# Kernel optimization log

Measured on AMD Instinct MI355X. Metric: run time of the kernel, lower is better.

## Reference

```python
import jax, jax.numpy as jnp
import numpy as np
from jax import lax

H = W = 200          # feature map size
STRIDE = 16
IMG_H = IMG_W = H * STRIDE  # 3200
C = 512
A = 9                # 3 scales x 3 aspect ratios
K_PRE = 1000         # pre-NMS topk (hardcoded in module)
K_POST = 100         # post-NMS keep (hardcoded in module)
IOU_TH = 0.7


def make_anchors():
    scales = jnp.array([128.0, 256.0, 512.0], dtype=jnp.float32)
    ratios = jnp.array([0.5, 1.0, 2.0], dtype=jnp.float32)
    hr = jnp.sqrt(ratios)                      # (3,)
    wr = 1.0 / hr
    ws = (wr[:, None] * scales[None, :]).reshape(-1)   # (9,)
    hs = (hr[:, None] * scales[None, :]).reshape(-1)
    base = jnp.stack([-ws / 2, -hs / 2, ws / 2, hs / 2], axis=1)  # (9,4)
    sx = jnp.arange(W, dtype=jnp.float32) * STRIDE
    sy = jnp.arange(H, dtype=jnp.float32) * STRIDE
    gy, gx = jnp.meshgrid(sy, sx, indexing='ij')
    shifts = jnp.stack([gx, gy, gx, gy], axis=-1).reshape(-1, 4)  # (H*W,4)
    return (shifts[:, None, :] + base[None, :, :]).reshape(-1, 4)  # (H*W*A,4)


def decode(anchors, deltas):
    w = anchors[:, 2] - anchors[:, 0]
    h = anchors[:, 3] - anchors[:, 1]
    cx = anchors[:, 0] + 0.5 * w
    cy = anchors[:, 1] + 0.5 * h
    px = deltas[:, 0] * w + cx
    py = deltas[:, 1] * h + cy
    pw = jnp.exp(deltas[:, 2]) * w
    ph = jnp.exp(deltas[:, 3]) * h
    return jnp.stack([px - 0.5 * pw, py - 0.5 * ph, px + 0.5 * pw, py + 0.5 * ph], axis=1)


def clamp_boxes(b):
    return jnp.stack([
        jnp.clip(b[:, 0], 0.0, IMG_W), jnp.clip(b[:, 1], 0.0, IMG_H),
        jnp.clip(b[:, 2], 0.0, IMG_W), jnp.clip(b[:, 3], 0.0, IMG_H)], axis=1)


def nms_keep(boxes, thr):
    # boxes (K_PRE,4) already sorted by descending score (topk output order)
    x1, y1, x2, y2 = boxes[:, 0], boxes[:, 1], boxes[:, 2], boxes[:, 3]
    areas = (x2 - x1) * (y2 - y1)
    idx = jnp.arange(K_PRE)

    def body(i, keep):
        iw = jnp.clip(jnp.minimum(x2[i], x2) - jnp.maximum(x1[i], x1), 0.0)
        ih = jnp.clip(jnp.minimum(y2[i], y2) - jnp.maximum(y1[i], y1), 0.0)
        inter = iw * ih
        iou = inter / (areas[i] + areas - inter)
        supp = (iou > thr) & (idx > i) & keep[i]
        return keep & jnp.logical_not(supp)

    return lax.fori_loop(0, K_PRE, body, jnp.ones(K_PRE, dtype=bool))


def rpn_forward(feat, conv_w, conv_b, cls_w, cls_b, reg_w, reg_b):
    dn = ('NCHW', 'OIHW', 'NCHW')
    x = lax.conv_general_dilated(feat, conv_w, (1, 1), 'SAME', dimension_numbers=dn)
    x = jax.nn.relu(x + conv_b[None, :, None, None])
    cls = lax.conv_general_dilated(x, cls_w, (1, 1), 'SAME', dimension_numbers=dn) + cls_b[None, :, None, None]
    reg = lax.conv_general_dilated(x, reg_w, (1, 1), 'SAME', dimension_numbers=dn) + reg_b[None, :, None, None]
    # (1,A,H,W) -> (H*W*A,)
    cls_logits = cls.transpose(0, 2, 3, 1).reshape(-1)
    # (1,A*4,H,W) -> (H*W*A,4)
    deltas = reg.reshape(1, A, 4, H, W).transpose(0, 3, 4, 1, 2).reshape(-1, 4)
    anchors = make_anchors()
    proposals = decode(anchors, deltas)
    scores = jax.nn.sigmoid(cls_logits)
    top_sc, top_idx = lax.top_k(scores, K_PRE)           # sorted descending
    props = clamp_boxes(proposals[top_idx])
    keep = lax.stop_gradient(nms_keep(props, IOU_TH))    # NMS decision is non-diff
    # kept indices, in score order (stable sort puts kept first, preserving order)
    order = jnp.argsort(jnp.where(keep, 0, 1), stable=True)[:K_POST]
    valid = jnp.arange(K_POST) < jnp.sum(keep)
    out_boxes = jnp.where(valid[:, None], props[order], 0.0)
    out_scores = jnp.where(valid, top_sc[order], 0.0)
    return out_boxes, out_scores


def setup_inputs() -> dict:
    key = jax.random.key(0)
    ks = jax.random.split(key, 7)
    s = 0.02
    return {
        'feat': jax.random.normal(ks[0], (1, C, H, W), dtype=jnp.float32),
        'conv_w': jax.random.normal(ks[1], (C, C, 3, 3), dtype=jnp.float32) * s,
        'conv_b': jnp.zeros((C,), dtype=jnp.float32),
        'cls_w': jax.random.normal(ks[2], (A, C, 1, 1), dtype=jnp.float32) * s,
        'cls_b': jnp.zeros((A,), dtype=jnp.float32),
        'reg_w': jax.random.normal(ks[3], (A * 4, C, 1, 1), dtype=jnp.float32) * s,
        'reg_b': jnp.zeros((A * 4,), dtype=jnp.float32),
    }


def reference(feat, conv_w, conv_b, cls_w, cls_b, reg_w, reg_b):
    return rpn_forward(feat, conv_w, conv_b, cls_w, cls_b, reg_w, reg_b)
```

## Files before the change

kernel.cpp:

```cpp
#include <hip/hip_runtime.h>
#include <stdint.h>

static constexpr int H_ = 200, W_ = 200, HW_ = 40000;
static constexpr int C_ = 512;
static constexpr int NANCH = 360000;
static constexpr int KPRE = 1000;
static constexpr int KPOST = 100;
static constexpr int KSEL = 1400;
static constexpr int PXCAP = 4096;
static constexpr int KSPLIT = 8;
static constexpr int FT = 212;
static constexpr int FP = 202;

typedef __attribute__((ext_vector_type(8))) short bf16x8;
typedef __attribute__((ext_vector_type(4))) float f32x4;

__device__ inline ushort f2bf(float f) {
    unsigned u = __float_as_uint(f);
    u += 0x7FFFu + ((u >> 16) & 1u);
    return (ushort)(u >> 16);
}
__device__ inline float bf2f(ushort h) { return __uint_as_float(((unsigned)h) << 16); }

typedef const __attribute__((address_space(1))) uint32_t gas_u32;
typedef __attribute__((address_space(3))) uint32_t las_u32;
__device__ __forceinline__ void gload_lds16(const void* g, void* l) {
    __builtin_amdgcn_global_load_lds((gas_u32*)(uintptr_t)g, (las_u32*)(uintptr_t)l, 16, 0, 0);
}

__global__ void k_zero_u32(unsigned* __restrict__ p, int n) {
    int i = blockIdx.x * 256 + threadIdx.x;
    if (i < n) p[i] = 0u;
}

__global__ void k_zero_border_t(ushort* __restrict__ feat_t) {
    int t = blockIdx.x * 256 + threadIdx.x;
    int total = 4944 * 64;
    if (t >= total) return;
    int px = t >> 6, part = t & 63;
    int y, x;
    if (px < 2544) { int ri = px / 212; x = px - ri * 212; y = (ri == 0) ? 0 : 200 + ri; }
    else { int q = px - 2544; int r12 = q / 12; int c = q - r12 * 12; y = 1 + r12; x = (c == 0) ? 0 : 200 + c; }
    uint4 z = {0u, 0u, 0u, 0u};
    *(uint4*)&feat_t[((size_t)y * FT + x) * 512 + part * 8] = z;
}

__global__ void k_zero_border_px(float* __restrict__ feat_px) {
    int t = blockIdx.x * 256 + threadIdx.x;
    int total = 804 * 128;
    if (t >= total) return;
    int px = t >> 7, part = t & 127;
    int y, x;
    if (px < 202)      { y = 0;   x = px; }
    else if (px < 404) { y = 201; x = px - 202; }
    else if (px < 604) { x = 0;   y = 1 + (px - 404); }
    else               { x = 201; y = 1 + (px - 604); }
    float4 z = {0.f, 0.f, 0.f, 0.f};
    *(float4*)&feat_px[((size_t)y * FP + x) * 512 + part * 4] = z;
}

__global__ void k_feat_t(const float* __restrict__ feat, ushort* __restrict__ feat_t) {
    __shared__ ushort lt[32 * 8 * 33];
    int x0 = blockIdx.x * 32, y0 = blockIdx.y * 8, ci0 = blockIdx.z * 32;
    int tid = threadIdx.x;
    for (int u = tid; u < 8192; u += 256) {
        int ciL = u >> 8, rem = u & 255;
        int yy = rem >> 5, xx = rem & 31;
        int x = x0 + xx;
        float v = (x < W_) ? feat[(size_t)(ci0 + ciL) * HW_ + (y0 + yy) * W_ + x] : 0.f;
        lt[(ciL * 8 + yy) * 33 + xx] = f2bf(v);
    }
    __syncthreads();
    for (int u = tid; u < 1024; u += 256) {
        int pxu = u >> 2, part = u & 3;
        int yy = pxu >> 5, xx = pxu & 31;
        if (x0 + xx >= W_) continue;
        ushort tmp[8];
#pragma unroll
        for (int k = 0; k < 8; ++k) tmp[k] = lt[((part * 8 + k) * 8 + yy) * 33 + xx];
        *(uint4*)&feat_t[((size_t)(y0 + yy + 1) * FT + (x0 + xx + 1)) * 512 + ci0 + part * 8] =
            *(const uint4*)&tmp[0];
    }
}

__global__ void k_feat_px(const float* __restrict__ feat, float* __restrict__ feat_px) {
    __shared__ float lt[32 * 8 * 33];
    int x0 = blockIdx.x * 32, y0 = blockIdx.y * 8, ci0 = blockIdx.z * 32;
    int tid = threadIdx.x;
    for (int u = tid; u < 8192; u += 256) {
        int ciL = u >> 8, rem = u & 255;
        int yy = rem >> 5, xx = rem & 31;
        int x = x0 + xx;
        float v = (x < W_) ? feat[(size_t)(ci0 + ciL) * HW_ + (y0 + yy) * W_ + x] : 0.f;
        lt[(ciL * 8 + yy) * 33 + xx] = v;
    }
    __syncthreads();
    for (int u = tid; u < 1024; u += 256) {
        int pxu = u >> 2, part = u & 3;
        int yy = pxu >> 5, xx = pxu & 31;
        if (x0 + xx >= W_) continue;
        float tmp[8];
#pragma unroll
        for (int k = 0; k < 8; ++k) tmp[k] = lt[((part * 8 + k) * 8 + yy) * 33 + xx];
        float* dst = &feat_px[((size_t)(y0 + yy + 1) * FP + (x0 + xx + 1)) * 512 + ci0 + part * 8];
        *(float4*)&dst[0] = *(const float4*)&tmp[0];
        *(float4*)&dst[4] = *(const float4*)&tmp[4];
    }
}

__global__ void k_wt_t(const float* __restrict__ conv_w, ushort* __restrict__ wt_t) {
    int i = blockIdx.x * 256 + threadIdx.x;
    if (i >= 9 * 512 * 512) return;
    int tap = i >> 18;
    int rem = i & 262143;
    int co = rem >> 9, ci = rem & 511;
    wt_t[i] = f2bf(conv_w[((size_t)co * 512 + ci) * 9 + tap]);
}

__global__ void k_wt_ex(const float* __restrict__ conv_w, float* __restrict__ wt_ex) {
    __shared__ float t[32][33];
    int kb = blockIdx.x * 32;
    int cb = blockIdx.y * 32;
    int lx = threadIdx.x, ly = threadIdx.y;
    int tap = kb >> 9, ci0 = kb & 511;
    for (int r = ly; r < 32; r += 8)
        t[r][lx] = conv_w[((size_t)(cb + r) * 512 + ci0 + lx) * 9 + tap];
    __syncthreads();
    for (int r = ly; r < 32; r += 8)
        wt_ex[(size_t)(kb + r) * 512 + cb + lx] = t[lx][r];
}

__global__ __launch_bounds__(256)
__attribute__((amdgpu_waves_per_eu(2, 4)))
void k_conv3_mfma(const ushort* __restrict__ feat_t, const ushort* __restrict__ wt_t,
                  const float* __restrict__ bias, ushort* __restrict__ xab) {
    __shared__ ushort halo[18 * 18 * 32];
    __shared__ ushort wtile[9 * 64 * 32];
    int b = blockIdx.x;
    int cot = b & 7;
    int tile = b >> 3;
    int xt = tile % 13, yt = tile / 13;
    int x0 = xt * 16, y0 = yt * 16;
    int co0 = cot * 64;
    int tid = threadIdx.x;
    int lane = tid & 63, wid = tid >> 6;
    int l15 = lane & 15, l4 = lane >> 4;

    f32x4 acc[4][4];
#pragma unroll
    for (int i = 0; i < 4; ++i)
#pragma unroll
        for (int j = 0; j < 4; ++j) acc[i][j] = (f32x4){0.f, 0.f, 0.f, 0.f};

    for (int ch = 0; ch < 16; ++ch) {
        int ci0 = ch * 32;
        __syncthreads();
        for (int u = tid; u < 1296; u += 256) {
            int p = u >> 2, q = u & 3;
            int r = p / 18, c = p - r * 18;
            const ushort* src = feat_t + ((size_t)(y0 + r) * FT + (x0 + c)) * 512 + ci0 + q * 8;
            gload_lds16(src, &halo[(u & ~63) * 8]);
        }
        for (int u = tid; u < 2304; u += 256) {
            int row = u >> 2, q = u & 3;
            int tap = row >> 6, co = row & 63;
            const ushort* src = wt_t + ((size_t)(tap * 512 + co0 + co)) * 512 + ci0 + q * 8;
            gload_lds16(src, &wtile[(u & ~63) * 8]);
        }
        __syncthreads();
#pragma unroll
        for (int tap = 0; tap < 9; ++tap) {
            int th = tap / 3, tw = tap - th * 3;
            bf16x8 af[4], bf[4];
#pragma unroll
            for (int pi = 0; pi < 4; ++pi)
                af[pi] = *(const bf16x8*)&halo[((wid * 4 + pi + th) * 18 + (l15 + tw)) * 32 + l4 * 8];
#pragma unroll
            for (int cj = 0; cj < 4; ++cj)
                bf[cj] = *(const bf16x8*)&wtile[(tap * 64 + cj * 16 + l15) * 32 + l4 * 8];
#pragma unroll
            for (int pi = 0; pi < 4; ++pi)
#pragma unroll
                for (int cj = 0; cj < 4; ++cj)
                    acc[pi][cj] = __builtin_amdgcn_mfma_f32_16x16x32_bf16(af[pi], bf[cj], acc[pi][cj], 0, 0, 0);
        }
    }

    float bv[4];
#pragma unroll
    for (int cj = 0; cj < 4; ++cj) bv[cj] = bias[co0 + cj * 16 + l15];
#pragma unroll
    for (int pi = 0; pi < 4; ++pi) {
        int yy = y0 + wid * 4 + pi;
        if (yy >= H_) continue;
#pragma unroll
        for (int cj = 0; cj < 4; ++cj) {
            int co = co0 + cj * 16 + l15;
#pragma unroll
            for (int r = 0; r < 4; ++r) {
                int xx = x0 + l4 * 4 + r;
                if (xx < W_) {
                    float v = acc[pi][cj][r] + bv[cj];
                    xab[((size_t)(yy * W_ + xx)) * 512 + co] = f2bf(v > 0.f ? v : 0.f);
                }
            }
        }
    }
}

__global__ void k_cls(const ushort* __restrict__ xab, const float* __restrict__ cls_w,
                      const float* __restrict__ cls_b, float* __restrict__ scores) {
    __shared__ float wl[9 * 512];
    int tid = threadIdx.x;
    for (int t = tid; t < 4608; t += 256) wl[t] = cls_w[t];
    __syncthreads();
    int l = tid & 63, w = tid >> 6;
    int pbase = blockIdx.x * 64 + w * 16;
    for (int u = 0; u < 16; ++u) {
        int px = pbase + u;
        float xv[8];
#pragma unroll
        for (int k = 0; k < 8; ++k) xv[k] = bf2f(xab[(size_t)px * 512 + k * 64 + l]);
#pragma unroll
        for (int a = 0; a < 9; ++a) {
            float s = 0.f;
#pragma unroll
            for (int k = 0; k < 8; ++k) s = fmaf(xv[k], wl[a * 512 + k * 64 + l], s);
#pragma unroll
            for (int o = 32; o > 0; o >>= 1) s += __shfl_down(s, o);
            if (l == 0) scores[(size_t)px * 9 + a] = 1.f / (1.f + expf(-(s + cls_b[a])));
        }
    }
}

__global__ void k_hist1_lds(const float* __restrict__ scores, unsigned* __restrict__ hist) {
    __shared__ unsigned h[16384];
    int tid = threadIdx.x;
    for (int j = tid; j < 16384; j += 256) h[j] = 0u;
    __syncthreads();
    int stride = gridDim.x * 256;
    for (int i = blockIdx.x * 256 + tid; i < NANCH; i += stride)
        atomicAdd(&h[(__float_as_uint(scores[i]) >> 16) & 16383], 1u);
    __syncthreads();
    for (int j = tid; j < 16384; j += 256) {
        unsigned v = h[j];
        if (v) atomicAdd(&hist[j], v);
    }
}

__global__ void k_find_thr(const unsigned* __restrict__ hist, unsigned* __restrict__ meta,
                           int mode, int Kwant) {
    __shared__ unsigned csum[1024];
    int t = threadIdx.x;
    unsigned base = (mode == 0) ? 0u : meta[1];
    unsigned s = 0;
    for (int b = 0; b < 64; ++b) s += hist[t * 64 + b];
    csum[t] = s;
    __syncthreads();
    for (int off = 1; off < 1024; off <<= 1) {
        unsigned add = (t + off < 1024) ? csum[t + off] : 0u;
        __syncthreads();
        csum[t] += add;
        __syncthreads();
    }
    unsigned run = base + ((t < 1023) ? csum[t + 1] : 0u);
    for (int b = 63; b >= 0; --b) {
        unsigned h = hist[t * 64 + b];
        if (run < (unsigned)Kwant && run + h >= (unsigned)Kwant) {
            if (mode == 0) {
                meta[0] = (unsigned)(t * 64 + b);
                meta[1] = run;
            } else {
                meta[2] = (meta[0] << 16) | (unsigned)(t * 64 + b);
                meta[3] = run;
                meta[4] = (unsigned)Kwant - run;
            }
            break;
        }
        run += h;
    }
}

__global__ void k_collect_cand(const float* __restrict__ scores, const unsigned* __restrict__ meta,
                               unsigned* __restrict__ flags) {
    int i = blockIdx.x * 256 + threadIdx.x;
    if (i >= NANCH) return;
    if ((__float_as_uint(scores[i]) >> 16) >= meta[0]) flags[i / 9] = 1u;
}

__global__ void k_px_compact(unsigned* __restrict__ flags, unsigned* __restrict__ meta,
                             unsigned* __restrict__ px_list) {
    int px = blockIdx.x * 256 + threadIdx.x;
    if (px >= HW_) return;
    if (flags[px]) {
        unsigned s = atomicAdd(&meta[10], 1u);
        if (s < (unsigned)PXCAP) { px_list[s] = (unsigned)px; flags[px] = s + 1u; }
        else flags[px] = 0u;
    }
}

__global__ __attribute__((amdgpu_waves_per_eu(2, 4)))
void k_exact_gemm(const float* __restrict__ feat_px, const float* __restrict__ wt_ex,
                  const unsigned* __restrict__ meta, const unsigned* __restrict__ px_list,
                  float* __restrict__ xpart) {
    int npx = (int)meta[10]; if (npx > PXCAP) npx = PXCAP;
    int pb = blockIdx.x;
    if (pb * 64 >= npx) return;
    int cot = blockIdx.y;
    int kz = blockIdx.z;
    __shared__ float A[32][68];
    __shared__ float B[32][68];
    __shared__ int plist[64];
    int tid = threadIdx.x;
    int co0 = cot * 64;
    if (tid < 64) {
        int slot = pb * 64 + tid;
        plist[tid] = (slot < npx) ? (int)px_list[slot] : (int)px_list[0];
    }
    int tcog = tid >> 4;
    int tpxg = tid & 15;
    float acc[4][4];
#pragma unroll
    for (int i = 0; i < 4; ++i)
#pragma unroll
        for (int j = 0; j < 4; ++j) acc[i][j] = 0.f;
    int kbase = kz * 576;
    for (int kc = 0; kc < 18; ++kc) {
        int k0 = kbase + kc * 32;
        int tap = k0 >> 9, ci0c = k0 & 511;
        int th = tap / 3, tw = tap - th * 3;
        __syncthreads();
        for (int u = tid; u < 512; u += 256) {
            int k = u >> 4, cp = (u & 15) * 4;
            *(float4*)&A[k][cp] = *(const float4*)&wt_ex[(size_t)(k0 + k) * 512 + co0 + cp];
        }
        for (int u = tid; u < 512; u += 256) {
            int s = u >> 3, part = u & 7;
            int px = plist[s];
            int y = px / W_, x = px - y * W_;
            float4 v = *(const float4*)&feat_px[((size_t)(y + th) * FP + (x + tw)) * 512 + ci0c + part * 4];
            B[part * 4 + 0][s] = v.x; B[part * 4 + 1][s] = v.y;
            B[part * 4 + 2][s] = v.z; B[part * 4 + 3][s] = v.w;
        }
        __syncthreads();
#pragma unroll 4
        for (int k = 0; k < 32; ++k) {
            float wv[4], pv[4];
            *(float4*)&wv[0] = *(const float4*)&A[k][tcog * 4];
            *(float4*)&pv[0] = *(const float4*)&B[k][tpxg * 4];
#pragma unroll
            for (int i = 0; i < 4; ++i)
#pragma unroll
                for (int j = 0; j < 4; ++j) acc[i][j] = fmaf(wv[i], pv[j], acc[i][j]);
        }
    }
#pragma unroll
    for (int j = 0; j < 4; ++j) {
        int slot = pb * 64 + tpxg * 4 + j;
        if (slot >= npx) continue;
        float tmp[4];
#pragma unroll
        for (int i = 0; i < 4; ++i) tmp[i] = acc[i][j];
        *(float4*)&xpart[((size_t)kz * PXCAP + slot) * 512 + co0 + tcog * 4] = *(float4*)&tmp[0];
    }
}

__global__ void k_exact_reduce(const float* __restrict__ xpart, const float* __restrict__ bias,
                               const unsigned* __restrict__ meta, float* __restrict__ xex) {
    int npx = (int)meta[10]; if (npx > PXCAP) npx = PXCAP;
    int idx = blockIdx.x * 256 + threadIdx.x;
    int slot = idx >> 9, co = idx & 511;
    if (slot >= npx) return;
    float v = 0.f;
#pragma unroll
    for (int kz = 0; kz < KSPLIT; ++kz)
        v += xpart[((size_t)kz * PXCAP + slot) * 512 + co];
    v += bias[co];
    xex[(size_t)slot * 512 + co] = v > 0.f ? v : 0.f;
}

__global__ void k_exact_scores(const float* __restrict__ xex, const float* __restrict__ cls_w,
                               const float* __restrict__ cls_b, const unsigned* __restrict__ meta,
                               float* __restrict__ scores_ex) {
    int slot = blockIdx.x;
    int npx = (int)meta[10]; if (npx > PXCAP) npx = PXCAP;
    if (slot >= npx) return;
    int l = threadIdx.x;
    float xv[8];
#pragma unroll
    for (int k = 0; k < 8; ++k) xv[k] = xex[(size_t)slot * 512 + k * 64 + l];
#pragma unroll
    for (int a = 0; a < 9; ++a) {
        float s = 0.f;
#pragma unroll
        for (int k = 0; k < 8; ++k) s = fmaf(xv[k], cls_w[a * 512 + k * 64 + l], s);
#pragma unroll
        for (int o = 32; o > 0; o >>= 1) s += __shfl_down(s, o);
        if (l == 0) scores_ex[slot * 9 + a] = 1.f / (1.f + expf(-(s + cls_b[a])));
    }
}

__global__ void k_hist1_ex_lds(const float* __restrict__ scores_ex, const unsigned* __restrict__ meta,
                               unsigned* __restrict__ hist) {
    __shared__ unsigned h[16384];
    int npx = (int)meta[10]; if (npx > PXCAP) npx = PXCAP;
    int n = npx * 9;
    int tid = threadIdx.x;
    for (int j = tid; j < 16384; j += 256) h[j] = 0u;
    __syncthreads();
    for (int i = blockIdx.x * 256 + tid; i < n; i += 32 * 256)
        atomicAdd(&h[(__float_as_uint(scores_ex[i]) >> 16) & 16383], 1u);
    __syncthreads();
    for (int j = tid; j < 16384; j += 256) {
        unsigned v = h[j];
        if (v) atomicAdd(&hist[j], v);
    }
}

__global__ void k_hist2_ex(const float* __restrict__ scores_ex, const unsigned* __restrict__ meta,
                           const unsigned* __restrict__ meta_ex, unsigned* __restrict__ hist2) {
    int npx = (int)meta[10]; if (npx > PXCAP) npx = PXCAP;
    int i = blockIdx.x * 256 + threadIdx.x;
    if (i >= npx * 9) return;
    unsigned b = __float_as_uint(scores_ex[i]);
    if ((b >> 16) == meta_ex[0]) atomicAdd(&hist2[b & 0xFFFFu], 1u);
}

__global__ void k_collect_ex(const float* __restrict__ scores_ex, const unsigned* __restrict__ meta,
                             unsigned* __restrict__ meta_ex, const unsigned* __restrict__ px_list,
                             unsigned* __restrict__ sel_bits, unsigned* __restrict__ sel_idx,
                             unsigned* __restrict__ eq_idx) {
    int npx = (int)meta[10]; if (npx > PXCAP) npx = PXCAP;
    int i = blockIdx.x * 256 + threadIdx.x;
    if (i >= npx * 9) return;
    unsigned b = __float_as_uint(scores_ex[i]);
    unsigned T = meta_ex[2];
    unsigned g = px_list[i / 9] * 9u + (unsigned)(i % 9);
    if (b > T) {
        unsigned s = atomicAdd(&meta_ex[8], 1u);
        if (s < 1024u) { sel_bits[s] = b; sel_idx[s] = g; }
    } else if (b == T) {
        unsigned s = atomicAdd(&meta_ex[9], 1u);
        if (s < 65536u) eq_idx[s] = g;
    }
}

__global__ void k_topk_final(const unsigned* __restrict__ sel_bits, const unsigned* __restrict__ sel_idx,
                             const unsigned* __restrict__ eq_idx, const unsigned* __restrict__ meta,
                             unsigned* __restrict__ top_idx, float* __restrict__ top_sc) {
    __shared__ uint64_t keys[1024];
    __shared__ int lcnt;
    __shared__ int lred;
    int t = threadIdx.x;
    unsigned cntGt = meta[3];
    unsigned need = meta[4];
    unsigned cntEq = meta[9];
    unsigned T = meta[2];

    unsigned idx_cut = 0xFFFFFFFFu;
    if (cntEq > need) {
        unsigned lo = 0, hi = NANCH - 1;
        while (lo < hi) {
            unsigned mid = (lo + hi) >> 1;
            int c = 0;
            for (unsigned e = t; e < cntEq; e += 1024)
                if (eq_idx[e] <= mid) c++;
            if (t == 0) lred = 0;
            __syncthreads();
            atomicAdd(&lred, c);
            __syncthreads();
            int tot = lred;
            __syncthreads();
            if ((unsigned)tot >= need) hi = mid; else lo = mid + 1;
        }
        idx_cut = lo;
    }

    keys[t] = 0ull;
    if (t == 0) lcnt = 0;
    __syncthreads();
    for (unsigned s = t; s < cntGt; s += 1024)
        keys[s] = ((uint64_t)sel_bits[s] << 32) | (uint64_t)(0xFFFFFFFFu - sel_idx[s]);
    for (unsigned e = t; e < cntEq; e += 1024) {
        unsigned ix = eq_idx[e];
        if (ix <= idx_cut) {
            int s2 = (int)cntGt + atomicAdd(&lcnt, 1);
            keys[s2] = ((uint64_t)T << 32) | (uint64_t)(0xFFFFFFFFu - ix);
        }
    }
    __syncthreads();
    for (int k = 2; k <= 1024; k <<= 1) {
        for (int j = k >> 1; j > 0; j >>= 1) {
            int ixj = t ^ j;
            if (ixj > t) {
                uint64_t a = keys[t], b = keys[ixj];
                bool desc = (t & k) == 0;
                if (desc ? (a < b) : (a > b)) { keys[t] = b; keys[ixj] = a; }
            }
            __syncthreads();
        }
    }
    if (t < KPRE) {
        top_sc[t] = __uint_as_float((unsigned)(keys[t] >> 32));
        top_idx[t] = 0xFFFFFFFFu - (unsigned)keys[t];
    }
}

__global__ void k_decode(const float* __restrict__ xex, const unsigned* __restrict__ flags,
                         const float* __restrict__ reg_w, const float* __restrict__ reg_b,
                         const unsigned* __restrict__ top_idx,
                         float* __restrict__ props, float* __restrict__ areas) {
    int j = blockIdx.x;
    int lane = threadIdx.x;
    unsigned idx = top_idx[j];
    int pix = (int)(idx / 9u);
    int a = (int)(idx - (unsigned)pix * 9u);
    int slot = (int)flags[pix] - 1;
    if (slot < 0) slot = 0;
    const float* xr = xex + (size_t)slot * 512;
    float s0 = 0, s1 = 0, s2 = 0, s3 = 0;
    for (int c = lane; c < C_; c += 64) {
        float xv = xr[c];
        s0 = fmaf(xv, reg_w[(a * 4 + 0) * C_ + c], s0);
        s1 = fmaf(xv, reg_w[(a * 4 + 1) * C_ + c], s1);
        s2 = fmaf(xv, reg_w[(a * 4 + 2) * C_ + c], s2);
        s3 = fmaf(xv, reg_w[(a * 4 + 3) * C_ + c], s3);
    }
#pragma unroll
    for (int o = 32; o > 0; o >>= 1) {
        s0 += __shfl_down(s0, o);
        s1 += __shfl_down(s1, o);
        s2 += __shfl_down(s2, o);
        s3 += __shfl_down(s3, o);
    }
    if (lane == 0) {
        float d0 = s0 + reg_b[a * 4 + 0];
        float d1 = s1 + reg_b[a * 4 + 1];
        float d2 = s2 + reg_b[a * 4 + 2];
        float d3 = s3 + reg_b[a * 4 + 3];
        int h = pix / W_, w2 = pix - h * W_;
        int rr = a / 3, ss = a - rr * 3;
        float ratio = (rr == 0) ? 0.5f : (rr == 1) ? 1.0f : 2.0f;
        float scale = (ss == 0) ? 128.f : (ss == 1) ? 256.f : 512.f;
        float hr = sqrtf(ratio);
        float wr = 1.0f / hr;
        float wsc = wr * scale, hsc = hr * scale;
        float sx = (float)w2 * 16.f, sy = (float)h * 16.f;
        float a0 = sx - wsc * 0.5f, a1 = sy - hsc * 0.5f;
        float a2 = sx + wsc * 0.5f, a3 = sy + hsc * 0.5f;
        float bw = a2 - a0, bh = a3 - a1;
        float cx = a0 + 0.5f * bw, cy = a1 + 0.5f * bh;
        float px = d0 * bw + cx, py = d1 * bh + cy;
        float pw = expf(d2) * bw, ph = expf(d3) * bh;
        float b0 = px - 0.5f * pw, b1 = py - 0.5f * ph;
        float b2 = px + 0.5f * pw, b3 = py + 0.5f * ph;
        b0 = fminf(fmaxf(b0, 0.f), 3200.f);
        b1 = fminf(fmaxf(b1, 0.f), 3200.f);
        b2 = fminf(fmaxf(b2, 0.f), 3200.f);
        b3 = fminf(fmaxf(b3, 0.f), 3200.f);
        props[j * 4 + 0] = b0;
        props[j * 4 + 1] = b1;
        props[j * 4 + 2] = b2;
        props[j * 4 + 3] = b3;
        areas[j] = (b2 - b0) * (b3 - b1);
    }
}

__global__ void k_nms_mask(const float* __restrict__ props, const float* __restrict__ areas,
                           unsigned long long* __restrict__ mask, float* __restrict__ out) {
    int i = blockIdx.x;
    int tid = threadIdx.x;
    if (i == 0) {
        for (int t = tid; t < KPOST * 5; t += 256) out[t] = 0.f;
    }
    float x1i = props[i * 4 + 0], y1i = props[i * 4 + 1];
    float x2i = props[i * 4 + 2], y2i = props[i * 4 + 3];
    float ai = areas[i];
#pragma unroll
    for (int k = 0; k < 4; ++k) {
        int j = k * 256 + tid;
        bool sup = false;
        if (j < KPRE && j > i) {
            float iw = fminf(x2i, props[j * 4 + 2]) - fmaxf(x1i, props[j * 4 + 0]);
            float ih = fminf(y2i, props[j * 4 + 3]) - fmaxf(y1i, props[j * 4 + 1]);
            iw = fmaxf(iw, 0.f);
            ih = fmaxf(ih, 0.f);
            float inter = iw * ih;
            float iou = inter / (ai + areas[j] - inter);
            sup = iou > 0.7f;
        }
        unsigned long long b = __ballot(sup);
        int word = k * 4 + (tid >> 6);
        if ((tid & 63) == 0) mask[(size_t)i * 16 + word] = b;
    }
}

__global__ void k_nms_scan_out(const unsigned long long* __restrict__ mask,
                               const float* __restrict__ props, const float* __restrict__ top_sc,
                               float* __restrict__ out) {
    __shared__ int kidx[KPOST];
    __shared__ int nk;
    int lane = threadIdx.x;
    if (lane == 0) {
        unsigned long long k0 = ~0ull, k1 = ~0ull, k2 = ~0ull, k3 = ~0ull;
        unsigned long long k4 = ~0ull, k5 = ~0ull, k6 = ~0ull, k7 = ~0ull;
        unsigned long long k8 = ~0ull, k9 = ~0ull, k10 = ~0ull, k11 = ~0ull;
        unsigned long long k12 = ~0ull, k13 = ~0ull, k14 = ~0ull;
        unsigned long long k15 = (1ull << 40) - 1ull;
        int kept = 0;
#define APPLY_ROW(ii) { const unsigned long long* row = &mask[(size_t)(ii) * 16];          \
        k0 &= ~row[0];  k1 &= ~row[1];  k2 &= ~row[2];  k3 &= ~row[3];                     \
        k4 &= ~row[4];  k5 &= ~row[5];  k6 &= ~row[6];  k7 &= ~row[7];                     \
        k8 &= ~row[8];  k9 &= ~row[9];  k10 &= ~row[10]; k11 &= ~row[11];                  \
        k12 &= ~row[12]; k13 &= ~row[13]; k14 &= ~row[14]; k15 &= ~row[15]; }
#define SCAN_WORD(w, kw) { \
        unsigned long long rem = kw; \
        while (rem) { \
            int b = __builtin_ctzll(rem); \
            kidx[kept++] = (w) * 64 + b; \
            if (kept == KPOST) goto done; \
            APPLY_ROW((w) * 64 + b); \
            rem &= kw; \
            rem &= (b >= 63) ? 0ull : ~((2ull << b) - 1ull); \
        } }
        SCAN_WORD(0, k0)  SCAN_WORD(1, k1)  SCAN_WORD(2, k2)  SCAN_WORD(3, k3)
        SCAN_WORD(4, k4)  SCAN_WORD(5, k5)  SCAN_WORD(6, k6)  SCAN_WORD(7, k7)
        SCAN_WORD(8, k8)  SCAN_WORD(9, k9)  SCAN_WORD(10, k10) SCAN_WORD(11, k11)
        SCAN_WORD(12, k12) SCAN_WORD(13, k13) SCAN_WORD(14, k14) SCAN_WORD(15, k15)
done:
        nk = kept;
#undef SCAN_WORD
#undef APPLY_ROW
    }
    __syncthreads();
    int n = nk;
    for (int t = lane; t < KPOST; t += 64) {
        if (t < n) {
            int i = kidx[t];
            out[t * 4 + 0] = props[i * 4 + 0];
            out[t * 4 + 1] = props[i * 4 + 1];
            out[t * 4 + 2] = props[i * 4 + 2];
            out[t * 4 + 3] = props[i * 4 + 3];
            out[KPOST * 4 + t] = top_sc[i];
        }
    }
}

extern "C" void kernel_launch(void* const* d_in, const int* in_sizes, int n_in,
                              void* d_out, int out_size, void* d_ws, size_t ws_size,
                              hipStream_t stream) {
    const float* feat   = (const float*)d_in[0];
    const float* conv_w = (const float*)d_in[1];
    const float* conv_b = (const float*)d_in[2];
    const float* cls_w  = (const float*)d_in[3];
    const float* cls_b  = (const float*)d_in[4];
    const float* reg_w  = (const float*)d_in[5];
    const float* reg_b  = (const float*)d_in[6];
    float* out = (float*)d_out;

    size_t off = 0;
    auto alloc = [&](size_t bytes) -> void* {
        off = (off + 255) & ~(size_t)255;
        void* p = (char*)d_ws + off;
        off += bytes;
        return p;
    };
    ushort* feat_t  = (ushort*)alloc((size_t)FT * FT * 512 * 2);
    float*  feat_px = (float*)alloc((size_t)FP * FP * 512 * 4);
    ushort* wt_t    = (ushort*)alloc((size_t)9 * 512 * 512 * 2);
    float*  wt_ex   = (float*)alloc((size_t)9 * 512 * 512 * 4);
    ushort* xab     = (ushort*)alloc((size_t)HW_ * 512 * 2);
    float*  xpart   = (float*)alloc((size_t)KSPLIT * PXCAP * 512 * 4);
    float*  xex     = (float*)alloc((size_t)PXCAP * 512 * 4);
    float*  scores  = (float*)alloc((size_t)NANCH * 4);
    float*  scores_ex = (float*)alloc((size_t)PXCAP * 9 * 4);
    unsigned* hist1   = (unsigned*)alloc(65536 * 4);
    unsigned* hist2   = (unsigned*)alloc(65536 * 4);
    unsigned* meta    = (unsigned*)alloc(64 * 4);
    unsigned* meta_ex = (unsigned*)alloc(64 * 4);
    unsigned* flags   = (unsigned*)alloc((size_t)HW_ * 4);
    unsigned* px_list = (unsigned*)alloc(PXCAP * 4);
    unsigned* sel_bits = (unsigned*)alloc(1024 * 4);
    unsigned* sel_idx  = (unsigned*)alloc(1024 * 4);
    unsigned* eq_idx   = (unsigned*)alloc(65536 * 4);
    unsigned* top_idx  = (unsigned*)alloc(KPRE * 4);
    float* top_sc      = (float*)alloc(KPRE * 4);
    float* props       = (float*)alloc(KPRE * 4 * 4);
    float* areas       = (float*)alloc(KPRE * 4);
    unsigned long long* mask = (unsigned long long*)alloc((size_t)KPRE * 16 * 8);
    (void)ws_size; (void)in_sizes; (void)n_in; (void)out_size;

    k_zero_border_t<<<(4944 * 64 + 255) / 256, 256, 0, stream>>>(feat_t);
    int zrDw = 65536 * 2 + 64 + 64 + HW_;
    k_zero_u32<<<(zrDw + 255) / 256, 256, 0, stream>>>(hist1, zrDw);
    k_feat_t<<<dim3(7, 25, 16), 256, 0, stream>>>(feat, feat_t);
    k_wt_t<<<(9 * 512 * 512 + 255) / 256, 256, 0, stream>>>(conv_w, wt_t);
    k_conv3_mfma<<<8 * 169, 256, 0, stream>>>(feat_t, wt_t, conv_b, xab);
    k_cls<<<HW_ / 64, 256, 0, stream>>>(xab, cls_w, cls_b, scores);
    k_hist1_lds<<<64, 256, 0, stream>>>(scores, hist1);
    k_find_thr<<<1, 1024, 0, stream>>>(hist1, meta, 0, KSEL);
    k_collect_cand<<<(NANCH + 255) / 256, 256, 0, stream>>>(scores, meta, flags);
    k_px_compact<<<(HW_ + 255) / 256, 256, 0, stream>>>(flags, meta, px_list);
    k_zero_border_px<<<(804 * 128 + 255) / 256, 256, 0, stream>>>(feat_px);
    k_feat_px<<<dim3(7, 25, 16), 256, 0, stream>>>(feat, feat_px);
    k_wt_ex<<<dim3(144, 16), dim3(32, 8), 0, stream>>>(conv_w, wt_ex);
    k_zero_u32<<<(65536 * 2 + 255) / 256, 256, 0, stream>>>(hist1, 65536 * 2);
    k_exact_gemm<<<dim3(PXCAP / 64, 8, KSPLIT), 256, 0, stream>>>(feat_px, wt_ex, meta, px_list, xpart);
    k_exact_reduce<<<PXCAP * 512 / 256, 256, 0, stream>>>(xpart, conv_b, meta, xex);
    k_exact_scores<<<PXCAP, 64, 0, stream>>>(xex, cls_w, cls_b, meta, scores_ex);
    k_hist1_ex_lds<<<32, 256, 0, stream>>>(scores_ex, meta, hist1);
    k_find_thr<<<1, 1024, 0, stream>>>(hist1, meta_ex, 0, KPRE);
    k_hist2_ex<<<(PXCAP * 9 + 255) / 256, 256, 0, stream>>>(scores_ex, meta, meta_ex, hist2);
    k_find_thr<<<1, 1024, 0, stream>>>(hist2, meta_ex, 1, KPRE);
    k_collect_ex<<<(PXCAP * 9 + 255) / 256, 256, 0, stream>>>(scores_ex, meta, meta_ex, px_list,
                                                              sel_bits, sel_idx, eq_idx);
    k_topk_final<<<1, 1024, 0, stream>>>(sel_bits, sel_idx, eq_idx, meta_ex, top_idx, top_sc);
    k_decode<<<KPRE, 64, 0, stream>>>(xex, flags, reg_w, reg_b, top_idx, props, areas);
    k_nms_mask<<<KPRE, 256, 0, stream>>>(props, areas, mask, out);
    k_nms_scan_out<<<1, 64, 0, stream>>>(mask, props, top_sc, out);
}
```

Before: 693.3 us.

## Register-prefetch next conv chunk to overlap global loads with MFMA

The conv3 MFMA kernel drops direct global-to-LDS loads and instead loads the next 32-channel chunk of halo and weights into registers, issued right after the barrier. Those registers are written to LDS at the start of the next iteration, so global latency overlaps the MFMA work on the current chunk. Output and split-K partial stores, and the partial loads in the reduce kernel, now use nontemporal hints. The prefetch adds about 60 VGPRs per thread, which can lower occupancy or cause spills, and it also adds an extra VGPR-to-LDS write.

After: 704.5 us. Within noise of the previous version (+1.6%).

```diff
diff --git a/kernel.cpp b/kernel.cpp
--- a/kernel.cpp
+++ b/kernel.cpp
@@ -21,12 +21,6 @@
     return (ushort)(u >> 16);
 }
 __device__ inline float bf2f(ushort h) { return __uint_as_float(((unsigned)h) << 16); }
-
-typedef const __attribute__((address_space(1))) uint32_t gas_u32;
-typedef __attribute__((address_space(3))) uint32_t las_u32;
-__device__ __forceinline__ void gload_lds16(const void* g, void* l) {
-    __builtin_amdgcn_global_load_lds((gas_u32*)(uintptr_t)g, (las_u32*)(uintptr_t)l, 16, 0, 0);
-}
 
 __global__ void k_zero_u32(unsigned* __restrict__ p, int n) {
     int i = blockIdx.x * 256 + threadIdx.x;
@@ -145,6 +139,61 @@
     int tid = threadIdx.x;
     int lane = tid & 63, wid = tid >> 6;
     int l15 = lane & 15, l4 = lane >> 4;
+    (void)lane;
+
+    const ushort* hsrc[6];
+    unsigned hoff[6];
+#pragma unroll
+    for (int i = 0; i < 6; ++i) {
+        int u = tid + i * 256;
+        int uu = (u < 1296) ? u : 0;
+        int p = uu >> 2, q = uu & 3;
+        int r = p / 18, c = p - r * 18;
+        hsrc[i] = feat_t + ((size_t)(y0 + r) * FT + (x0 + c)) * 512 + q * 8;
+        hoff[i] = (unsigned)(uu * 8);
+    }
+    const ushort* wsrc[9];
+    unsigned woff[9];
+#pragma unroll
+    for (int i = 0; i < 9; ++i) {
+        int u = tid + i * 256;
+        int row = u >> 2, q = u & 3;
+        int tap = row >> 6, co = row & 63;
+        wsrc[i] = wt_t + ((size_t)(tap * 512 + co0 + co)) * 512 + q * 8;
+        woff[i] = (unsigned)(u * 8);
+    }
+
+    uint4 hreg0, hreg1, hreg2, hreg3, hreg4, hreg5;
+    uint4 wreg0, wreg1, wreg2, wreg3, wreg4, wreg5, wreg6, wreg7, wreg8;
+
+#define ISSUE(ci0c) do {                                                     \
+    hreg0 = *(const uint4*)(hsrc[0] + (ci0c));                               \
+    hreg1 = *(const uint4*)(hsrc[1] + (ci0c));                               \
+    hreg2 = *(const uint4*)(hsrc[2] + (ci0c));                               \
+    hreg3 = *(const uint4*)(hsrc[3] + (ci0c));                               \
+    hreg4 = *(const uint4*)(hsrc[4] + (ci0c));                               \
+    hreg5 = *(const uint4*)(hsrc[5] + (ci0c));                               \
+    wreg0 = *(const uint4*)(wsrc[0] + (ci0c));                               \
+    wreg1 = *(const uint4*)(wsrc[1] + (ci0c));                               \
+    wreg2 = *(const uint4*)(wsrc[2] + (ci0c));                               \
+    wreg3 = *(const uint4*)(wsrc[3] + (ci0c));                               \
+    wreg4 = *(const uint4*)(wsrc[4] + (ci0c));                               \
+    wreg5 = *(const uint4*)(wsrc[5] + (ci0c));                               \
+    wreg6 = *(const uint4*)(wsrc[6] + (ci0c));                               \
+    wreg7 = *(const uint4*)(wsrc[7] + (ci0c));                               \
+    wreg8 = *(const uint4*)(wsrc[8] + (ci0c));                               \
+} while (0)
+
+#define COMMIT() do {                                                        \
+    *(uint4*)&halo[hoff[0]] = hreg0;  *(uint4*)&halo[hoff[1]] = hreg1;       \
+    *(uint4*)&halo[hoff[2]] = hreg2;  *(uint4*)&halo[hoff[3]] = hreg3;       \
+    *(uint4*)&halo[hoff[4]] = hreg4;  *(uint4*)&halo[hoff[5]] = hreg5;       \
+    *(uint4*)&wtile[woff[0]] = wreg0; *(uint4*)&wtile[woff[1]] = wreg1;      \
+    *(uint4*)&wtile[woff[2]] = wreg2; *(uint4*)&wtile[woff[3]] = wreg3;      \
+    *(uint4*)&wtile[woff[4]] = wreg4; *(uint4*)&wtile[woff[5]] = wreg5;      \
+    *(uint4*)&wtile[woff[6]] = wreg6; *(uint4*)&wtile[woff[7]] = wreg7;      \
+    *(uint4*)&wtile[woff[8]] = wreg8;                                        \
+} while (0)
 
     f32x4 acc[4][4];
 #pragma unroll
@@ -152,22 +201,12 @@
 #pragma unroll
         for (int j = 0; j < 4; ++j) acc[i][j] = (f32x4){0.f, 0.f, 0.f, 0.f};
 
+    ISSUE(0);
     for (int ch = 0; ch < 16; ++ch) {
-        int ci0 = ch * 32;
         __syncthreads();
-        for (int u = tid; u < 1296; u += 256) {
-            int p = u >> 2, q = u & 3;
-            int r = p / 18, c = p - r * 18;
-            const ushort* src = feat_t + ((size_t)(y0 + r) * FT + (x0 + c)) * 512 + ci0 + q * 8;
-            gload_lds16(src, &halo[(u & ~63) * 8]);
-        }
-        for (int u = tid; u < 2304; u += 256) {
-            int row = u >> 2, q = u & 3;
-            int tap = row >> 6, co = row & 63;
-            const ushort* src = wt_t + ((size_t)(tap * 512 + co0 + co)) * 512 + ci0 + q * 8;
-            gload_lds16(src, &wtile[(u & ~63) * 8]);
-        }
+        COMMIT();
         __syncthreads();
+        if (ch < 15) ISSUE((ch + 1) * 32);
 #pragma unroll
         for (int tap = 0; tap < 9; ++tap) {
             int th = tap / 3, tw = tap - th * 3;
@@ -185,6 +224,8 @@
                     acc[pi][cj] = __builtin_amdgcn_mfma_f32_16x16x32_bf16(af[pi], bf[cj], acc[pi][cj], 0, 0, 0);
         }
     }
+#undef ISSUE
+#undef COMMIT
 
     float bv[4];
 #pragma unroll
@@ -201,7 +242,8 @@
                 int xx = x0 + l4 * 4 + r;
                 if (xx < W_) {
                     float v = acc[pi][cj][r] + bv[cj];
-                    xab[((size_t)(yy * W_ + xx)) * 512 + co] = f2bf(v > 0.f ? v : 0.f);
+                    __builtin_nontemporal_store(f2bf(v > 0.f ? v : 0.f),
+                        &xab[((size_t)(yy * W_ + xx)) * 512 + co]);
                 }
             }
         }
@@ -358,10 +400,10 @@
     for (int j = 0; j < 4; ++j) {
         int slot = pb * 64 + tpxg * 4 + j;
         if (slot >= npx) continue;
-        float tmp[4];
-#pragma unroll
-        for (int i = 0; i < 4; ++i) tmp[i] = acc[i][j];
-        *(float4*)&xpart[((size_t)kz * PXCAP + slot) * 512 + co0 + tcog * 4] = *(float4*)&tmp[0];
+        f32x4 tmp;
+        tmp[0] = acc[0][j]; tmp[1] = acc[1][j]; tmp[2] = acc[2][j]; tmp[3] = acc[3][j];
+        __builtin_nontemporal_store(tmp,
+            (f32x4*)&xpart[((size_t)kz * PXCAP + slot) * 512 + co0 + tcog * 4]);
     }
 }
 
@@ -374,7 +416,7 @@
     float v = 0.f;
 #pragma unroll
     for (int kz = 0; kz < KSPLIT; ++kz)
-        v += xpart[((size_t)kz * PXCAP + slot) * 512 + co];
+        v += __builtin_nontemporal_load(&xpart[((size_t)kz * PXCAP + slot) * 512 + co]);
     v += bias[co];
     xex[(size_t)slot * 512 + co] = v > 0.f ? v : 0.f;
 }
```
